# Kernel optimization log

Hardware: AMD Instinct MI355X
Metric: run time of the kernel (lower is better)

The kernel has to match this reference:

```python
import jax, jax.numpy as jnp
import numpy as np

DIM = 1024      # dim
FW = 14         # focal_window
FL = 2          # focal_level
FF = 4          # focal_factor


def _dwconv_gelu(x, w, b):
    # x: [B, C, S], w: [C, 1, k] depthwise kernel, torch 'same' padding
    k = w.shape[-1]
    y = jax.lax.conv_general_dilated(
        x, w, window_strides=(1,), padding=[((k - 1) // 2, k // 2)],
        feature_group_count=x.shape[1], dimension_numbers=('NCH', 'OIH', 'NCH'))
    return jax.nn.gelu(y + b[None, :, None], approximate=False)


def setup_inputs() -> dict:
    key = jax.random.key(0)
    ks = jax.random.split(key, 8)
    B, S, D = 8, 4096, DIM
    P = 2 * D + FL + 1  # 2051
    s = 0.02
    return {
        'input': jax.random.normal(ks[0], (B, S, D), jnp.float32),
        'W_in': jax.random.normal(ks[1], (D, P), jnp.float32) * s,
        'b_in': jnp.zeros((P,), jnp.float32),
        'w0': jax.random.normal(ks[2], (D, 1, FW), jnp.float32) * s,
        'b0': jnp.zeros((D,), jnp.float32),
        'w1': jax.random.normal(ks[3], (D, 1, FF + FW), jnp.float32) * s,  # kernel 18
        'b1': jnp.zeros((D,), jnp.float32),
        'W_ctx': jax.random.normal(ks[4], (D, D), jnp.float32) * s,
        'b_ctx': jnp.zeros((D,), jnp.float32),
        'W_out': jax.random.normal(ks[5], (D, D), jnp.float32) * s,
        'b_out': jnp.zeros((D,), jnp.float32),
    }


def reference(input, W_in, b_in, w0, b0, w1, b1, W_ctx, b_ctx, W_out, b_out):
    D = DIM
    # in_proj then permute to channel-first [B, 2D+FL+1, S]
    proj = (input @ W_in + b_in).transpose(0, 2, 1)
    query = proj[:, :D]            # [B, D, S]
    ctx = proj[:, D:2 * D]         # [B, D, S]
    gates = proj[:, 2 * D:]        # [B, FL+1, S]
    # hierarchical depthwise conv pyramid (context fed through successive levels)
    c0 = _dwconv_gelu(ctx, w0, b0)
    c1 = _dwconv_gelu(c0, w1, b1)
    context_all = c0 * gates[:, 0:1] + c1 * gates[:, 1:2]
    # global context branch
    g = jax.nn.gelu(c1.mean(axis=-1), approximate=False)  # [B, D]
    context_all = context_all + g[..., None] * gates[:, FL:FL + 1]
    # context_proj is a 1x1 conv == per-position linear over channels
    modulator = jnp.einsum('oc,bcs->bos', W_ctx, context_all) + b_ctx[None, :, None]
    out = (query * modulator).transpose(0, 2, 1)  # [B, S, D]
    return out @ W_out + b_out
```

## Files before the change

kernel.cpp:

```cpp
#include <hip/hip_runtime.h>

#define DIMC 1024
#define BATCH 8
#define SEQ 4096
#define BS (BATCH*SEQ)
#define PCOL 2051

typedef unsigned short ushort_t;
typedef __attribute__((ext_vector_type(8))) short short8;
typedef __attribute__((ext_vector_type(4))) float f32x4;
typedef __attribute__((ext_vector_type(4))) unsigned short us4;

__device__ __forceinline__ float bf2f(ushort_t u) {
    union { unsigned u32; float f; } v; v.u32 = ((unsigned)u) << 16; return v.f;
}
__device__ __forceinline__ ushort_t f2bf(float f) {
    union { float f; unsigned u; } v; v.f = f;
    unsigned r = v.u + 0x7fffu + ((v.u >> 16) & 1u);
    return (ushort_t)(r >> 16);
}
__device__ __forceinline__ float gelu_exact(float x) {
    return 0.5f * x * (1.0f + erff(x * 0.7071067811865475f));
}
__device__ __forceinline__ void gld16(const ushort_t* g, ushort_t* l) {
    __builtin_amdgcn_global_load_lds(
        (const __attribute__((address_space(1))) unsigned int*)g,
        (__attribute__((address_space(3))) unsigned int*)l, 16, 0, 0);
}

__global__ void cvt_f32_bf16(const float* __restrict__ src, ushort_t* __restrict__ dst, int n) {
    int i = (blockIdx.x * 256 + threadIdx.x) * 4;
    if (i >= n) return;
    f32x4 v = *(const f32x4*)(src + i);
    us4 o;
    #pragma unroll
    for (int j = 0; j < 4; j++) o[j] = f2bf(v[j]);
    *(us4*)(dst + i) = o;
}

__global__ void transpose_cvt(const float* __restrict__ src, ushort_t* __restrict__ dst,
                              int ld, int K) {
    __shared__ float tile[32][33];
    int tx = threadIdx.x & 31, ty = threadIdx.x >> 5;
    int n0 = blockIdx.x * 32, k0 = blockIdx.y * 32;
    #pragma unroll
    for (int j = 0; j < 4; j++)
        tile[ty + j * 8][tx] = src[(size_t)(k0 + ty + j * 8) * ld + n0 + tx];
    __syncthreads();
    #pragma unroll
    for (int j = 0; j < 4; j++)
        dst[(size_t)(n0 + ty + j * 8) * K + k0 + tx] = f2bf(tile[tx][ty + j * 8]);
}

__global__ void pack_gatesw(const float* __restrict__ W_in, float* __restrict__ wg) {
    int d = blockIdx.x * 256 + threadIdx.x;
    if (d >= 1024) return;
    const float* p = W_in + (size_t)d * PCOL + 2048;
    wg[d] = p[0]; wg[1024 + d] = p[1]; wg[2048 + d] = p[2];
}

__global__ void cvt_gates(const float* __restrict__ input, const float* __restrict__ wg,
                          const float* __restrict__ b_in, ushort_t* __restrict__ ibf,
                          float* __restrict__ gates) {
    int row = blockIdx.x, tid = threadIdx.x;
    int lane = tid & 63, wave = tid >> 6;
    size_t base = (size_t)row * 1024 + tid * 4;
    f32x4 v = *(const f32x4*)(input + base);
    us4 o;
    #pragma unroll
    for (int j = 0; j < 4; j++) o[j] = f2bf(v[j]);
    *(us4*)(ibf + base) = o;
    f32x4 w0v = *(const f32x4*)(wg + tid * 4);
    f32x4 w1v = *(const f32x4*)(wg + 1024 + tid * 4);
    f32x4 w2v = *(const f32x4*)(wg + 2048 + tid * 4);
    float a0 = 0, a1 = 0, a2 = 0;
    #pragma unroll
    for (int j = 0; j < 4; j++) { a0 += v[j] * w0v[j]; a1 += v[j] * w1v[j]; a2 += v[j] * w2v[j]; }
    #pragma unroll
    for (int off = 32; off; off >>= 1) {
        a0 += __shfl_down(a0, off, 64);
        a1 += __shfl_down(a1, off, 64);
        a2 += __shfl_down(a2, off, 64);
    }
    __shared__ float red[4][3];
    if (lane == 0) { red[wave][0] = a0; red[wave][1] = a1; red[wave][2] = a2; }
    __syncthreads();
    if (tid == 0) {
        gates[row * 4 + 0] = red[0][0] + red[1][0] + red[2][0] + red[3][0] + b_in[2048];
        gates[row * 4 + 1] = red[0][1] + red[1][1] + red[2][1] + red[3][1] + b_in[2049];
        gates[row * 4 + 2] = red[0][2] + red[1][2] + red[2][2] + red[3][2] + b_in[2050];
    }
}

template<int MODE>
__global__ __launch_bounds__(256, 2)
void gemm_bt(const ushort_t* __restrict__ A, const ushort_t* __restrict__ Bt,
             const float* __restrict__ bias, void* __restrict__ C,
             const ushort_t* __restrict__ Q, const float* __restrict__ gates,
             const float* __restrict__ vb, int K, int ldc, int ldq) {
    __shared__ ushort_t lA[128 * 32];
    __shared__ ushort_t lB[128 * 32];
    const int tid = threadIdx.x, lane = tid & 63, wave = tid >> 6;
    const int bn = blockIdx.x, bm = blockIdx.y;
    const int wm = (wave >> 1) * 64, wn = (wave & 1) * 64;
    const int lr = lane & 15, kq = (lane >> 4) * 8;

    const ushort_t* Ag = A + (size_t)bm * 128 * K;
    const ushort_t* Bg = Bt + (size_t)bn * 128 * K;

    f32x4 acc[4][4];
    #pragma unroll
    for (int i = 0; i < 4; i++)
        #pragma unroll
        for (int j = 0; j < 4; j++)
            #pragma unroll
            for (int r = 0; r < 4; r++) acc[i][j][r] = 0.0f;

    for (int k0 = 0; k0 < K; k0 += 32) {
        #pragma unroll
        for (int i = 0; i < 2; i++) {
            int cb = i * 256 + wave * 64;
            int c  = cb + lane;
            int row = c >> 2, kk = (c & 3) << 3;
            gld16(Ag + (size_t)row * K + kk, &lA[cb << 3]);
            gld16(Bg + (size_t)row * K + kk, &lB[cb << 3]);
        }
        Ag += 32; Bg += 32;
        __syncthreads();

        short8 af[4], bfr[4];
        #pragma unroll
        for (int mt = 0; mt < 4; mt++)
            af[mt] = *(const short8*)&lA[(wm + mt * 16 + lr) * 32 + kq];
        #pragma unroll
        for (int nt = 0; nt < 4; nt++)
            bfr[nt] = *(const short8*)&lB[(wn + nt * 16 + lr) * 32 + kq];
        #pragma unroll
        for (int mt = 0; mt < 4; mt++)
            #pragma unroll
            for (int nt = 0; nt < 4; nt++)
                acc[mt][nt] = __builtin_amdgcn_mfma_f32_16x16x32_bf16(
                    af[mt], bfr[nt], acc[mt][nt], 0, 0, 0);
        __syncthreads();
    }

    const int lq = lane >> 4;
    const int bbatch = (bm * 128) >> 12;
    #pragma unroll
    for (int mt = 0; mt < 4; mt++) {
        #pragma unroll
        for (int r = 0; r < 4; r++) {
            int row = bm * 128 + wm + mt * 16 + lq * 4 + r;
            size_t rowc = (size_t)row * ldc;
            float g2;
            if (MODE == 1) g2 = gates[row * 4 + 2];
            #pragma unroll
            for (int nt = 0; nt < 4; nt++) {
                int col = bn * 128 + wn + nt * 16 + lr;
                float v = acc[mt][nt][r] + bias[col];
                if (MODE == 1) {
                    v += g2 * vb[bbatch * 1024 + col];
                    v *= bf2f(Q[(size_t)row * ldq + col]);
                }
                if (MODE == 2) ((float*)C)[rowc + col] = v;
                else           ((ushort_t*)C)[rowc + col] = f2bf(v);
            }
        }
    }
}

__global__ __launch_bounds__(256)
void dwconv_fused(const ushort_t* __restrict__ proj,
                  const float* __restrict__ w0, const float* __restrict__ b0,
                  const float* __restrict__ w1, const float* __restrict__ b1,
                  const float* __restrict__ gates,
                  ushort_t* __restrict__ P, float* __restrict__ G) {
    __shared__ float xc[94 * 64];
    __shared__ float x0[81 * 64];
    __shared__ float gl[2][64];
    __shared__ float rs[256];
    const int tid = threadIdx.x;
    const int s0 = blockIdx.x * 64, d0 = blockIdx.y * 64, b = blockIdx.z;
    for (int c = tid; c < 94 * 8; c += 256) {
        int r = c >> 3, dd = (c & 7) * 8;
        int s = s0 - 14 + r;
        float f[8];
        if (s >= 0 && s < SEQ) {
            short8 u = *(const short8*)&proj[(size_t)(b * SEQ + s) * 2048 + 1024 + d0 + dd];
            #pragma unroll
            for (int j = 0; j < 8; j++) f[j] = bf2f((ushort_t)u[j]);
        } else {
            #pragma unroll
            for (int j = 0; j < 8; j++) f[j] = 0.f;
        }
        f32x4 v0 = {f[0], f[1], f[2], f[3]}, v1 = {f[4], f[5], f[6], f[7]};
        *(f32x4*)&xc[r * 64 + dd] = v0;
        *(f32x4*)&xc[r * 64 + dd + 4] = v1;
    }
    if (tid < 64) gl[0][tid] = gates[(size_t)(b * SEQ + s0 + tid) * 4 + 0];
    else if (tid < 128) gl[1][tid - 64] = gates[(size_t)(b * SEQ + s0 + tid - 64) * 4 + 1];
    const int d = tid & 63, sc = tid >> 6;
    float wr0[14], wr1[18];
    #pragma unroll
    for (int t = 0; t < 14; t++) wr0[t] = w0[(size_t)(d0 + d) * 14 + t];
    float bb0 = b0[d0 + d];
    #pragma unroll
    for (int t = 0; t < 18; t++) wr1[t] = w1[(size_t)(d0 + d) * 18 + t];
    float bb1 = b1[d0 + d];
    __syncthreads();
    {
        float xw[34];
        int r0 = sc * 20;
        #pragma unroll
        for (int r = 0; r < 34; r++) xw[r] = xc[(r0 + r) * 64 + d];
        #pragma unroll
        for (int i = 0; i < 21; i++) {
            int rr = r0 + i;
            int s = s0 - 8 + rr;
            float acc = bb0;
            #pragma unroll
            for (int t = 0; t < 14; t++) acc += wr0[t] * xw[i + t];
            x0[rr * 64 + d] = (s >= 0 && s < SEQ) ? gelu_exact(acc) : 0.f;
        }
    }
    __syncthreads();
    float xw1[33];
    #pragma unroll
    for (int r = 0; r < 33; r++) xw1[r] = x0[(sc * 16 + r) * 64 + d];
    float psum = 0.f;
    #pragma unroll
    for (int i = 0; i < 16; i++) {
        float acc = bb1;
        #pragma unroll
        for (int t = 0; t < 18; t++) acc += wr1[t] * xw1[i + t];
        float c1 = gelu_exact(acc);
        psum += c1;
        float c0v = xw1[i + 8];
        int sl = sc * 16 + i;
        float pv = c0v * gl[0][sl] + c1 * gl[1][sl];
        P[(size_t)(b * SEQ + s0 + sl) * 1024 + d0 + d] = f2bf(pv);
    }
    rs[tid] = psum;
    __syncthreads();
    if (sc == 0)
        atomicAdd(&G[b * 1024 + d0 + d], rs[d] + rs[64 + d] + rs[128 + d] + rs[192 + d]);
}

__global__ __launch_bounds__(256)
void gemv_v(const float* __restrict__ G, const ushort_t* __restrict__ wctxB,
            float* __restrict__ v) {
    __shared__ float gg[1024];
    const int tid = threadIdx.x, b = blockIdx.y;
    for (int i = tid; i < 1024; i += 256)
        gg[i] = gelu_exact(G[b * 1024 + i] * (1.0f / (float)SEQ));
    __syncthreads();
    const int w = tid >> 6, lane = tid & 63;
    const int o = blockIdx.x * 4 + w;
    const ushort_t* wr = wctxB + (size_t)o * 1024;
    float acc = 0.f;
    #pragma unroll
    for (int j = 0; j < 16; j++)
        acc += gg[j * 64 + lane] * bf2f(wr[j * 64 + lane]);
    #pragma unroll
    for (int off = 32; off; off >>= 1) acc += __shfl_down(acc, off, 64);
    if (lane == 0) v[b * 1024 + o] = acc;
}

extern "C" void kernel_launch(void* const* d_in, const int* in_sizes, int n_in,
                              void* d_out, int out_size, void* d_ws, size_t ws_size,
                              hipStream_t stream) {
    const float* input = (const float*)d_in[0];
    const float* W_in  = (const float*)d_in[1];
    const float* b_in  = (const float*)d_in[2];
    const float* w0    = (const float*)d_in[3];
    const float* b0    = (const float*)d_in[4];
    const float* w1    = (const float*)d_in[5];
    const float* b1    = (const float*)d_in[6];
    const float* W_ctx = (const float*)d_in[7];
    const float* b_ctx = (const float*)d_in[8];
    const float* W_out = (const float*)d_in[9];
    const float* b_out = (const float*)d_in[10];

    char* ws = (char*)d_ws;
    size_t o = 0;
    ushort_t* ibf   = (ushort_t*)(ws + o); o += (size_t)BS * 1024 * 2;
    ushort_t* proj  = (ushort_t*)(ws + o); o += (size_t)BS * 2048 * 2;
    ushort_t* Y     = (ushort_t*)(ws + o); o += (size_t)BS * 1024 * 2;
    float*    gates = (float*)   (ws + o); o += (size_t)BS * 4 * 4;
    float*    G     = (float*)   (ws + o); o += (size_t)BATCH * 1024 * 4;
    float*    v     = (float*)   (ws + o); o += (size_t)BATCH * 1024 * 4;
    float*    wg    = (float*)   (ws + o); o += (size_t)3 * 1024 * 4;
    ushort_t* winT  = (ushort_t*)(ws + o); o += (size_t)2048 * 1024 * 2;
    ushort_t* wctxB = (ushort_t*)(ws + o); o += (size_t)1024 * 1024 * 2;
    ushort_t* woutT = (ushort_t*)(ws + o); o += (size_t)1024 * 1024 * 2;
    ushort_t* P = ibf;

    hipMemsetAsync(G, 0, BATCH * 1024 * sizeof(float), stream);
    pack_gatesw<<<4, 256, 0, stream>>>(W_in, wg);
    transpose_cvt<<<dim3(2048 / 32, 1024 / 32), 256, 0, stream>>>(W_in, winT, PCOL, 1024);
    cvt_f32_bf16<<<1024 * 1024 / 4 / 256, 256, 0, stream>>>(W_ctx, wctxB, 1024 * 1024);
    transpose_cvt<<<dim3(1024 / 32, 1024 / 32), 256, 0, stream>>>(W_out, woutT, 1024, 1024);
    cvt_gates<<<BS, 256, 0, stream>>>(input, wg, b_in, ibf, gates);
    gemm_bt<0><<<dim3(16, 256), 256, 0, stream>>>(ibf, winT, b_in, proj, nullptr, nullptr, nullptr, 1024, 2048, 0);
    dwconv_fused<<<dim3(SEQ / 64, 16, BATCH), 256, 0, stream>>>(proj, w0, b0, w1, b1, gates, P, G);
    gemv_v<<<dim3(256, BATCH), 256, 0, stream>>>(G, wctxB, v);
    gemm_bt<1><<<dim3(8, 256), 256, 0, stream>>>(P, wctxB, b_ctx, Y, proj, gates, v, 1024, 1024, 2048);
    gemm_bt<2><<<dim3(8, 256), 256, 0, stream>>>(Y, woutT, b_out, d_out, nullptr, nullptr, nullptr, 1024, 1024, 0);
}
```

Before: 736.7 us.

## Replace 128x128 GEMM with 256x256 double-buffered pipelined MFMA kernel

Replaces the 128x128-tile, 256-thread GEMM with a 256x256-tile, 512-thread kernel using a K-step of 64. It double-buffers LDS with staged global-to-LDS loads interleaved across four MFMA phases, and uses explicit barriers, waitcnt and setprio. It also swizzles the LDS layout to avoid bank conflicts and remaps workgroups per XCD for cache locality. The aim is more data reuse per tile and better overlap of memory with MFMA. In exchange it uses 128KB of LDS and higher register pressure, and the hand-tuned sync must stay correct.

```diff
diff --git a/kernel.cpp b/kernel.cpp
--- a/kernel.cpp
+++ b/kernel.cpp
@@ -93,70 +93,123 @@
 }
 
 template<int MODE>
-__global__ __launch_bounds__(256, 2)
-void gemm_bt(const ushort_t* __restrict__ A, const ushort_t* __restrict__ Bt,
+__global__ __launch_bounds__(512, 2)
+void gemm256(const ushort_t* __restrict__ A, const ushort_t* __restrict__ Bt,
              const float* __restrict__ bias, void* __restrict__ C,
              const ushort_t* __restrict__ Q, const float* __restrict__ gates,
-             const float* __restrict__ vb, int K, int ldc, int ldq) {
-    __shared__ ushort_t lA[128 * 32];
-    __shared__ ushort_t lB[128 * 32];
+             const float* __restrict__ vb, int K, int ldc, int ldq, int nbx) {
+    __shared__ ushort_t lA[2][16384];
+    __shared__ ushort_t lB[2][16384];
     const int tid = threadIdx.x, lane = tid & 63, wave = tid >> 6;
-    const int bn = blockIdx.x, bm = blockIdx.y;
-    const int wm = (wave >> 1) * 64, wn = (wave & 1) * 64;
-    const int lr = lane & 15, kq = (lane >> 4) * 8;
-
-    const ushort_t* Ag = A + (size_t)bm * 128 * K;
-    const ushort_t* Bg = Bt + (size_t)bn * 128 * K;
-
-    f32x4 acc[4][4];
-    #pragma unroll
-    for (int i = 0; i < 4; i++)
+    const int lr = lane & 15, kq = lane >> 4;
+    const int wrm = wave >> 2, wrn = wave & 3;
+
+    const int nwg = gridDim.x, bid = blockIdx.x;
+    const int q8 = nwg >> 3, r8 = nwg & 7;
+    const int xcd = bid & 7, linb = bid >> 3;
+    const int wgid = (xcd < r8 ? xcd * (q8 + 1) : r8 * (q8 + 1) + (xcd - r8) * q8) + linb;
+    const int bn = wgid % nbx, bm = wgid / nbx;
+
+    const ushort_t* Ag = A + (size_t)bm * 256 * K;
+    const ushort_t* Bg = Bt + (size_t)bn * 256 * K;
+
+    const int xsw = kq ^ (((lr >> 3) & 1) << 1);
+    const int fBase = lr * 32 + xsw * 8;
+
+    int srOff[2][2], ldsC[2][2];
+    #pragma unroll
+    for (int h = 0; h < 2; h++)
+        #pragma unroll
+        for (int j = 0; j < 2; j++) {
+            int c = h * 1024 + j * 512 + tid;
+            int sub = c >> 6, rl = (c >> 2) & 15, cc = c & 3;
+            int r  = ((sub >> 1) << 4) | rl;
+            int k8 = ((sub & 1) << 2) | (cc ^ (((rl >> 3) & 1) << 1));
+            srOff[h][j] = r * K + k8 * 8;
+            ldsC[h][j]  = (h * 1024 + j * 512 + (wave << 6)) << 3;
+        }
+
+    f32x4 acc[8][4];
+    #pragma unroll
+    for (int i = 0; i < 8; i++)
         #pragma unroll
         for (int j = 0; j < 4; j++)
             #pragma unroll
-            for (int r = 0; r < 4; r++) acc[i][j][r] = 0.0f;
-
-    for (int k0 = 0; k0 < K; k0 += 32) {
-        #pragma unroll
-        for (int i = 0; i < 2; i++) {
-            int cb = i * 256 + wave * 64;
-            int c  = cb + lane;
-            int row = c >> 2, kk = (c & 3) << 3;
-            gld16(Ag + (size_t)row * K + kk, &lA[cb << 3]);
-            gld16(Bg + (size_t)row * K + kk, &lB[cb << 3]);
-        }
-        Ag += 32; Bg += 32;
-        __syncthreads();
-
-        short8 af[4], bfr[4];
-        #pragma unroll
-        for (int mt = 0; mt < 4; mt++)
-            af[mt] = *(const short8*)&lA[(wm + mt * 16 + lr) * 32 + kq];
-        #pragma unroll
-        for (int nt = 0; nt < 4; nt++)
-            bfr[nt] = *(const short8*)&lB[(wn + nt * 16 + lr) * 32 + kq];
-        #pragma unroll
-        for (int mt = 0; mt < 4; mt++)
-            #pragma unroll
-            for (int nt = 0; nt < 4; nt++)
-                acc[mt][nt] = __builtin_amdgcn_mfma_f32_16x16x32_bf16(
-                    af[mt], bfr[nt], acc[mt][nt], 0, 0, 0);
-        __syncthreads();
-    }
-
-    const int lq = lane >> 4;
-    const int bbatch = (bm * 128) >> 12;
-    #pragma unroll
-    for (int mt = 0; mt < 4; mt++) {
+            for (int r = 0; r < 4; r++) acc[i][j][r] = 0.f;
+
+    short8 af[2][2], bfr[4][2];
+
+#define STG(ARR, bb, G, kt, h) do { \
+    gld16((G) + (size_t)(kt) * 64 + srOff[h][0], &ARR[bb][ldsC[h][0]]); \
+    gld16((G) + (size_t)(kt) * 64 + srOff[h][1], &ARR[bb][ldsC[h][1]]); \
+} while (0)
+
+#define PHASE(bb, qq, STAGE_STMT, DOVM) do { \
+    if ((qq) == 0) { \
+        _Pragma("unroll") \
+        for (int nt = 0; nt < 4; nt++) { \
+            bfr[nt][0] = *(const short8*)&lB[bb][fBase + ((wrn * 4 + nt) * 2 + 0) * 512]; \
+            bfr[nt][1] = *(const short8*)&lB[bb][fBase + ((wrn * 4 + nt) * 2 + 1) * 512]; \
+        } \
+    } \
+    af[0][0] = *(const short8*)&lA[bb][fBase + ((wrm * 8 + (qq) * 2 + 0) * 2 + 0) * 512]; \
+    af[0][1] = *(const short8*)&lA[bb][fBase + ((wrm * 8 + (qq) * 2 + 0) * 2 + 1) * 512]; \
+    af[1][0] = *(const short8*)&lA[bb][fBase + ((wrm * 8 + (qq) * 2 + 1) * 2 + 0) * 512]; \
+    af[1][1] = *(const short8*)&lA[bb][fBase + ((wrm * 8 + (qq) * 2 + 1) * 2 + 1) * 512]; \
+    STAGE_STMT; \
+    __builtin_amdgcn_s_barrier(); \
+    asm volatile("s_waitcnt lgkmcnt(0)" ::: "memory"); \
+    __builtin_amdgcn_s_setprio(1); \
+    _Pragma("unroll") \
+    for (int mi = 0; mi < 2; mi++) \
+        _Pragma("unroll") \
+        for (int nt = 0; nt < 4; nt++) { \
+            acc[(qq) * 2 + mi][nt] = __builtin_amdgcn_mfma_f32_16x16x32_bf16( \
+                af[mi][0], bfr[nt][0], acc[(qq) * 2 + mi][nt], 0, 0, 0); \
+            acc[(qq) * 2 + mi][nt] = __builtin_amdgcn_mfma_f32_16x16x32_bf16( \
+                af[mi][1], bfr[nt][1], acc[(qq) * 2 + mi][nt], 0, 0, 0); \
+        } \
+    __builtin_amdgcn_s_setprio(0); \
+    if (DOVM) asm volatile("s_waitcnt vmcnt(4)" ::: "memory"); \
+    __builtin_amdgcn_s_barrier(); \
+} while (0)
+
+    STG(lA, 0, Ag, 0, 0); STG(lA, 0, Ag, 0, 1);
+    STG(lB, 0, Bg, 0, 0); STG(lB, 0, Bg, 0, 1);
+    STG(lB, 1, Bg, 1, 0); STG(lB, 1, Bg, 1, 1);
+    asm volatile("s_waitcnt vmcnt(4)" ::: "memory");
+    __builtin_amdgcn_s_barrier();
+
+    const int KT = K >> 6;
+    for (int it = 0; it < (K >> 7); it++) {
+        int t1 = 2 * it + 1;
+        int t2 = 2 * it + 2; if (t2 > KT - 1) t2 = KT - 1;
+        int t3 = 2 * it + 3; if (t3 > KT - 1) t3 = KT - 1;
+        PHASE(0, 0, STG(lA, 1, Ag, t1, 0), 0);
+        PHASE(0, 1, STG(lA, 1, Ag, t1, 1), 0);
+        PHASE(0, 2, STG(lB, 0, Bg, t2, 0), 0);
+        PHASE(0, 3, STG(lB, 0, Bg, t2, 1), 1);
+        PHASE(1, 0, STG(lA, 0, Ag, t2, 0), 0);
+        PHASE(1, 1, STG(lA, 0, Ag, t2, 1), 0);
+        PHASE(1, 2, STG(lB, 1, Bg, t3, 0), 0);
+        PHASE(1, 3, STG(lB, 1, Bg, t3, 1), 1);
+    }
+#undef PHASE
+#undef STG
+    asm volatile("s_waitcnt vmcnt(0)" ::: "memory");
+
+    const int bbatch = (bm * 256) >> 12;
+    #pragma unroll
+    for (int mt = 0; mt < 8; mt++) {
         #pragma unroll
         for (int r = 0; r < 4; r++) {
-            int row = bm * 128 + wm + mt * 16 + lq * 4 + r;
+            int row = bm * 256 + wrm * 128 + mt * 16 + kq * 4 + r;
             size_t rowc = (size_t)row * ldc;
             float g2;
             if (MODE == 1) g2 = gates[row * 4 + 2];
             #pragma unroll
             for (int nt = 0; nt < 4; nt++) {
-                int col = bn * 128 + wn + nt * 16 + lr;
+                int col = bn * 256 + wrn * 64 + nt * 16 + lr;
                 float v = acc[mt][nt][r] + bias[col];
                 if (MODE == 1) {
                     v += g2 * vb[bbatch * 1024 + col];
@@ -301,9 +354,12 @@
     cvt_f32_bf16<<<1024 * 1024 / 4 / 256, 256, 0, stream>>>(W_ctx, wctxB, 1024 * 1024);
     transpose_cvt<<<dim3(1024 / 32, 1024 / 32), 256, 0, stream>>>(W_out, woutT, 1024, 1024);
     cvt_gates<<<BS, 256, 0, stream>>>(input, wg, b_in, ibf, gates);
-    gemm_bt<0><<<dim3(16, 256), 256, 0, stream>>>(ibf, winT, b_in, proj, nullptr, nullptr, nullptr, 1024, 2048, 0);
+    gemm256<0><<<dim3(8 * (BS / 256)), 512, 0, stream>>>(ibf, winT, b_in, proj,
+        nullptr, nullptr, nullptr, 1024, 2048, 0, 8);
     dwconv_fused<<<dim3(SEQ / 64, 16, BATCH), 256, 0, stream>>>(proj, w0, b0, w1, b1, gates, P, G);
     gemv_v<<<dim3(256, BATCH), 256, 0, stream>>>(G, wctxB, v);
-    gemm_bt<1><<<dim3(8, 256), 256, 0, stream>>>(P, wctxB, b_ctx, Y, proj, gates, v, 1024, 1024, 2048);
-    gemm_bt<2><<<dim3(8, 256), 256, 0, stream>>>(Y, woutT, b_out, d_out, nullptr, nullptr, nullptr, 1024, 1024, 0);
-}
+    gemm256<1><<<dim3(4 * (BS / 256)), 512, 0, stream>>>(P, wctxB, b_ctx, Y,
+        proj, gates, v, 1024, 1024, 2048, 4);
+    gemm256<2><<<dim3(4 * (BS / 256)), 512, 0, stream>>>(Y, woutT, b_out, d_out,
+        nullptr, nullptr, nullptr, 1024, 1024, 0, 4);
+}
```

Result: faster. 660.8 us (-10.3%).
